# Kernel tuning notes

Hardware: AMD Instinct MI355X
Metric: run time of the kernel (lower is better)

Reference implementation:

```python
import jax, jax.numpy as jnp
import numpy as np

D = 1024
H = 16
HD = D // H
FF = 4 * D
EPS = 1e-5


def setup_inputs() -> dict:
    key = jax.random.key(0)
    ks = jax.random.split(key, 16)
    s = lambda k, shape, scale: jax.random.normal(k, shape, dtype=jnp.float32) * scale
    inp = {
        "x": s(ks[0], (8, 1024, D), 1.0),
        "Wq": s(ks[1], (D, D), D ** -0.5), "bq": jnp.zeros((D,), jnp.float32),
        "Wk": s(ks[2], (D, D), D ** -0.5), "bk": jnp.zeros((D,), jnp.float32),
        "Wv": s(ks[3], (D, D), D ** -0.5), "bv": jnp.zeros((D,), jnp.float32),
        "Wo": s(ks[4], (D, D), D ** -0.5), "bo": jnp.zeros((D,), jnp.float32),
        "W1": s(ks[5], (D, FF), D ** -0.5), "b1": jnp.zeros((FF,), jnp.float32),
        "W2": s(ks[6], (FF, D), FF ** -0.5), "b2": jnp.zeros((D,), jnp.float32),
        "g1": jnp.ones((D,), jnp.float32), "be1": jnp.zeros((D,), jnp.float32),
        "g2": jnp.ones((D,), jnp.float32), "be2": jnp.zeros((D,), jnp.float32),
    }
    return inp


def _layernorm(x, g, b):
    mu = jnp.mean(x, axis=-1, keepdims=True)
    var = jnp.var(x, axis=-1, keepdims=True)
    return (x - mu) * jax.lax.rsqrt(var + EPS) * g + b


def reference(x, Wq, bq, Wk, bk, Wv, bv, Wo, bo, W1, b1, W2, b2, g1, be1, g2, be2):
    B, S, _ = x.shape
    # --- pre-norm attention block (dropout = identity in eval) ---
    h = _layernorm(x, g1, be1)
    q = (h @ Wq + bq).reshape(B, S, H, HD)
    k = (h @ Wk + bk).reshape(B, S, H, HD)
    v = (h @ Wv + bv).reshape(B, S, H, HD)
    scores = jnp.einsum('bqhd,bkhd->bhqk', q, k) / jnp.sqrt(jnp.float32(HD))
    attn = jax.nn.softmax(scores, axis=-1)
    ctx = jnp.einsum('bhqk,bkhd->bqhd', attn, v).reshape(B, S, D)
    x = x + (ctx @ Wo + bo)
    # --- pre-norm FFN block ---
    h = _layernorm(x, g2, be2)
    h = jax.nn.gelu(h @ W1 + b1, approximate=False)
    x = x + (h @ W2 + b2)
    return x
```

## Files before the change

kernel.cpp:

```cpp
#include <hip/hip_runtime.h>
#include <hip/hip_bf16.h>
#include <math.h>
#include <stdint.h>

typedef unsigned short u16;
typedef unsigned int u32;
typedef __attribute__((ext_vector_type(8))) short short8;
typedef __attribute__((ext_vector_type(4))) float f32x4;

__device__ __forceinline__ float b2f(u16 u) {
  union { u32 i; float f; } v; v.i = ((u32)u) << 16; return v.f;
}
__device__ __forceinline__ u16 f2b(float f) {
  union { float f; u32 i; } v; v.f = f;
  return (u16)((v.i + 0x7FFFu + ((v.i >> 16) & 1u)) >> 16);
}

__device__ __forceinline__ void gload_lds16(const u16* g, u16* l) {
  __builtin_amdgcn_global_load_lds((const __attribute__((address_space(1))) void*)g,
                                   (__attribute__((address_space(3))) void*)l, 16, 0, 0);
}

__global__ __launch_bounds__(256) void transpose_k(const float* __restrict__ in,
                                                   u16* __restrict__ out, int K, int N) {
  __shared__ u16 tile[32][33];
  int n0 = blockIdx.x * 32, k0 = blockIdx.y * 32;
  int tx = threadIdx.x & 31, ty = threadIdx.x >> 5;
  #pragma unroll
  for (int i = ty; i < 32; i += 8)
    tile[i][tx] = f2b(in[(size_t)(k0 + i) * N + n0 + tx]);
  __syncthreads();
  #pragma unroll
  for (int i = ty; i < 32; i += 8)
    out[(size_t)(n0 + i) * K + k0 + tx] = tile[tx][i];
}

__global__ __launch_bounds__(256) void vtrans_k(const u16* __restrict__ v, u16* __restrict__ vt) {
  __shared__ u16 tile[32][33];
  int bh = blockIdx.y, b = bh >> 4, h = bh & 15;
  int s0 = (blockIdx.x & 31) * 32, d0 = (blockIdx.x >> 5) * 32;
  int tx = threadIdx.x & 31, ty = threadIdx.x >> 5;
  #pragma unroll
  for (int i = ty; i < 32; i += 8)
    tile[i][tx] = v[(size_t)(b * 1024 + s0 + i) * 1024 + h * 64 + d0 + tx];
  __syncthreads();
  #pragma unroll
  for (int i = ty; i < 32; i += 8)
    vt[(size_t)(bh * 64 + d0 + i) * 1024 + s0 + tx] = tile[tx][i];
}

template<int FP32IN>
__global__ __launch_bounds__(256) void ln_k(const void* __restrict__ xv, const float* __restrict__ g,
                                            const float* __restrict__ be, u16* __restrict__ out) {
  int row = blockIdx.x, t = threadIdx.x;
  float f0, f1, f2, f3;
  if (FP32IN) {
    const float* xr = (const float*)xv + (size_t)row * 1024;
    float4 x4 = *(const float4*)(xr + t * 4);
    f0 = x4.x; f1 = x4.y; f2 = x4.z; f3 = x4.w;
  } else {
    const u16* xr = (const u16*)xv + (size_t)row * 1024;
    ushort4 x4 = *(const ushort4*)(xr + t * 4);
    f0 = b2f(x4.x); f1 = b2f(x4.y); f2 = b2f(x4.z); f3 = b2f(x4.w);
  }
  float s = f0 + f1 + f2 + f3;
  float ss = f0 * f0 + f1 * f1 + f2 * f2 + f3 * f3;
  #pragma unroll
  for (int off = 32; off > 0; off >>= 1) { s += __shfl_down(s, off); ss += __shfl_down(ss, off); }
  __shared__ float sb[4], ssb[4];
  if ((t & 63) == 0) { sb[t >> 6] = s; ssb[t >> 6] = ss; }
  __syncthreads();
  s = sb[0] + sb[1] + sb[2] + sb[3];
  ss = ssb[0] + ssb[1] + ssb[2] + ssb[3];
  float mu = s * (1.0f / 1024.0f);
  float var = ss * (1.0f / 1024.0f) - mu * mu;
  float rstd = rsqrtf(var + 1e-5f);
  float4 gv = *(const float4*)(g + t * 4);
  float4 bv = *(const float4*)(be + t * 4);
  ushort4 o;
  o.x = f2b((f0 - mu) * rstd * gv.x + bv.x);
  o.y = f2b((f1 - mu) * rstd * gv.y + bv.y);
  o.z = f2b((f2 - mu) * rstd * gv.z + bv.z);
  o.w = f2b((f3 - mu) * rstd * gv.w + bv.w);
  *(ushort4*)(out + (size_t)row * 1024 + t * 4) = o;
}

template<int ACT, int RESID, int OUTF32>
__global__ __launch_bounds__(256) void gemm_k(const u16* __restrict__ A, const u16* __restrict__ Bt,
                                              const float* __restrict__ bias, const void* __restrict__ resid,
                                              void* __restrict__ Cv, int M, int N, int K) {
  __shared__ u16 As[2][128 * 32];
  __shared__ u16 Bs[2][128 * 32];
  int n0 = blockIdx.x * 128, m0 = blockIdx.y * 128;
  int t = threadIdx.x;
  int wave = t >> 6, lane = t & 63, quad = lane >> 4, l16 = lane & 15;
  int wm = (wave >> 1) * 64, wn = (wave & 1) * 64;
  f32x4 acc[4][4] = {};
  int lr = lane >> 2;
  int lc = (lane & 3) ^ (lr & 3);
  const u16* Ab = A + (size_t)(m0 + wave * 16 + lr) * K + lc * 8;
  const u16* Bb = Bt + (size_t)(n0 + wave * 16 + lr) * K + lc * 8;
  const int lb = wave * 16 * 32;
  const int rdoff = (quad ^ (l16 & 3)) * 8;
  #pragma unroll
  for (int i = 0; i < 2; i++) {
    gload_lds16(Ab + (size_t)i * 64 * K, &As[0][lb + i * 64 * 32]);
    gload_lds16(Bb + (size_t)i * 64 * K, &Bs[0][lb + i * 64 * 32]);
  }
  const int niter = K >> 5;
  for (int c = 0; c < niter; c++) {
    int buf = c & 1;
    __syncthreads();
    if (c + 1 < niter) {
      int k1 = (c + 1) << 5;
      #pragma unroll
      for (int i = 0; i < 2; i++) {
        gload_lds16(Ab + k1 + (size_t)i * 64 * K, &As[buf ^ 1][lb + i * 64 * 32]);
        gload_lds16(Bb + k1 + (size_t)i * 64 * K, &Bs[buf ^ 1][lb + i * 64 * 32]);
      }
    }
    short8 a[4], b[4];
    #pragma unroll
    for (int i = 0; i < 4; i++)
      a[i] = *(const short8*)(&As[buf][(wm + i * 16 + l16) * 32 + rdoff]);
    #pragma unroll
    for (int j = 0; j < 4; j++)
      b[j] = *(const short8*)(&Bs[buf][(wn + j * 16 + l16) * 32 + rdoff]);
    #pragma unroll
    for (int i = 0; i < 4; i++)
      #pragma unroll
      for (int j = 0; j < 4; j++)
        acc[i][j] = __builtin_amdgcn_mfma_f32_16x16x32_bf16(a[i], b[j], acc[i][j], 0, 0, 0);
  }
  float bcol[4];
  #pragma unroll
  for (int j = 0; j < 4; j++) bcol[j] = bias[n0 + wn + j * 16 + l16];
  #pragma unroll
  for (int i = 0; i < 4; i++) {
    #pragma unroll
    for (int r = 0; r < 4; r++) {
      int row = m0 + wm + i * 16 + quad * 4 + r;
      #pragma unroll
      for (int j = 0; j < 4; j++) {
        int col = n0 + wn + j * 16 + l16;
        float v = acc[i][j][r] + bcol[j];
        if (ACT == 1) {
          float e = v * (2.3022082f + 0.1029431f * v * v);
          float tt = exp2f(fminf(e, 80.0f));
          v = v * tt / (tt + 1.0f);
        }
        if (RESID == 1) v += b2f(((const u16*)resid)[(size_t)row * N + col]);
        if (RESID == 2) v += ((const float*)resid)[(size_t)row * N + col];
        if (OUTF32) ((float*)Cv)[(size_t)row * N + col] = v;
        else        ((u16*)Cv)[(size_t)row * N + col] = f2b(v);
      }
    }
  }
}

__global__ __launch_bounds__(256) void attn_k(const u16* __restrict__ Q, const u16* __restrict__ Kb,
                                              const u16* __restrict__ VT, u16* __restrict__ ctx) {
  int bh = blockIdx.x;
  int b = bh >> 4;
  int q0 = blockIdx.y * 64;
  int t = threadIdx.x, wave = t >> 6, lane = t & 63, quad = lane >> 4, l16 = lane & 15;
  __shared__ u16 Ks[2][64 * 64];
  __shared__ u16 Vs[2][64 * 64];
  __shared__ u16 Plds[4][16][72];
  const size_t base = ((size_t)b * 1024) * 1024 + (size_t)(bh & 15) * 64;
  const u16* Kbase = Kb + base;
  const u16* vtb = VT + (size_t)bh * 64 * 1024;
  int lrow = lane >> 3;
  int lchunk = (lane & 7) ^ (lrow & 7);
  int srow = wave * 16;
  short8 qa[2];
  #pragma unroll
  for (int kh = 0; kh < 2; kh++)
    qa[kh] = *(const short8*)(Q + base + (size_t)(q0 + wave * 16 + l16) * 1024 + kh * 32 + quad * 8);
  #pragma unroll
  for (int half = 0; half < 2; half++) {
    int r8 = srow + half * 8;
    gload_lds16(Kbase + (size_t)(r8 + lrow) * 1024 + lchunk * 8, &Ks[0][r8 * 64]);
    gload_lds16(vtb + (size_t)(r8 + lrow) * 1024 + lchunk * 8, &Vs[0][r8 * 64]);
  }
  f32x4 o[4] = {};
  float l_acc[4] = {0.f, 0.f, 0.f, 0.f};
  for (int c = 0; c < 16; c++) {
    int buf = c & 1;
    __syncthreads();
    if (c < 15) {
      #pragma unroll
      for (int half = 0; half < 2; half++) {
        int r8 = srow + half * 8;
        gload_lds16(Kbase + (size_t)((c + 1) * 64 + r8 + lrow) * 1024 + lchunk * 8, &Ks[buf ^ 1][r8 * 64]);
        gload_lds16(vtb + (size_t)(r8 + lrow) * 1024 + (c + 1) * 64 + lchunk * 8, &Vs[buf ^ 1][r8 * 64]);
      }
    }
    f32x4 s[4] = {};
    #pragma unroll
    for (int kh = 0; kh < 2; kh++)
      #pragma unroll
      for (int j = 0; j < 4; j++) {
        int row = j * 16 + l16;
        int pc = (kh * 4 + quad) ^ (row & 7);
        short8 kb = *(const short8*)(&Ks[buf][row * 64 + pc * 8]);
        s[j] = __builtin_amdgcn_mfma_f32_16x16x32_bf16(qa[kh], kb, s[j], 0, 0, 0);
      }
    #pragma unroll
    for (int j = 0; j < 4; j++)
      #pragma unroll
      for (int r = 0; r < 4; r++) {
        float p = exp2f(s[j][r] * 0.18033688011112042f);
        l_acc[r] += p;
        Plds[wave][quad * 4 + r][j * 16 + l16] = f2b(p);
      }
    #pragma unroll
    for (int kh = 0; kh < 2; kh++) {
      short8 pa = *(const short8*)(&Plds[wave][l16][kh * 32 + quad * 8]);
      #pragma unroll
      for (int d4 = 0; d4 < 4; d4++) {
        int row = d4 * 16 + l16;
        int pc = (kh * 4 + quad) ^ (row & 7);
        short8 vb = *(const short8*)(&Vs[buf][row * 64 + pc * 8]);
        o[d4] = __builtin_amdgcn_mfma_f32_16x16x32_bf16(pa, vb, o[d4], 0, 0, 0);
      }
    }
  }
  #pragma unroll
  for (int off = 1; off < 16; off <<= 1)
    #pragma unroll
    for (int r = 0; r < 4; r++) l_acc[r] += __shfl_xor(l_acc[r], off);
  #pragma unroll
  for (int r = 0; r < 4; r++) {
    float inv = 1.0f / l_acc[r];
    size_t row = (size_t)b * 1024 + q0 + wave * 16 + quad * 4 + r;
    #pragma unroll
    for (int d4 = 0; d4 < 4; d4++) {
      int col = (bh & 15) * 64 + d4 * 16 + l16;
      ctx[row * 1024 + col] = f2b(o[d4][r] * inv);
    }
  }
}

extern "C" void kernel_launch(void* const* d_in, const int* in_sizes, int n_in,
                              void* d_out, int out_size, void* d_ws, size_t ws_size,
                              hipStream_t stream) {
  const float* x   = (const float*)d_in[0];
  const float* Wq  = (const float*)d_in[1];  const float* bq  = (const float*)d_in[2];
  const float* Wk  = (const float*)d_in[3];  const float* bk  = (const float*)d_in[4];
  const float* Wv  = (const float*)d_in[5];  const float* bv  = (const float*)d_in[6];
  const float* Wo  = (const float*)d_in[7];  const float* bo  = (const float*)d_in[8];
  const float* W1  = (const float*)d_in[9];  const float* b1  = (const float*)d_in[10];
  const float* W2  = (const float*)d_in[11]; const float* b2  = (const float*)d_in[12];
  const float* g1  = (const float*)d_in[13]; const float* be1 = (const float*)d_in[14];
  const float* g2  = (const float*)d_in[15]; const float* be2 = (const float*)d_in[16];

  char* ws = (char*)d_ws;
  const size_t MB = 1024 * 1024;
  const bool full = ws_size >= 144 * MB;
  u16* R0  = (u16*)(ws + 0 * MB);
  u16* R1  = (u16*)(ws + 16 * MB);
  u16* R2  = (u16*)(ws + 32 * MB);
  u16* WqT = (u16*)(ws + 48 * MB);
  u16* WkT = (u16*)(ws + 50 * MB);
  u16* WvT = (u16*)(ws + 52 * MB);
  u16* WoT = (u16*)(ws + 54 * MB);
  u16* W1T = full ? (u16*)(ws + 64 * MB) : (u16*)(ws + 56 * MB);
  u16* W2T = full ? (u16*)(ws + 72 * MB) : R2;
  u16* h3f = (u16*)(ws + 80 * MB);
  float* out = (float*)d_out;
  u16* vb  = (u16*)d_out;
  u16* ctx = (u16*)d_out;
  u16* h2  = full ? R2 : (u16*)d_out + (size_t)8192 * 1024;
  u16* vt  = R0;

  transpose_k<<<dim3(32, 32), 256, 0, stream>>>(Wq, WqT, 1024, 1024);
  transpose_k<<<dim3(32, 32), 256, 0, stream>>>(Wk, WkT, 1024, 1024);
  transpose_k<<<dim3(32, 32), 256, 0, stream>>>(Wv, WvT, 1024, 1024);
  transpose_k<<<dim3(32, 32), 256, 0, stream>>>(Wo, WoT, 1024, 1024);
  transpose_k<<<dim3(128, 32), 256, 0, stream>>>(W1, W1T, 1024, 4096);
  if (full) transpose_k<<<dim3(32, 128), 256, 0, stream>>>(W2, W2T, 4096, 1024);

  ln_k<1><<<8192, 256, 0, stream>>>(x, g1, be1, R0);

  gemm_k<0, 0, 0><<<dim3(8, 64), 256, 0, stream>>>(R0, WqT, bq, nullptr, R1, 8192, 1024, 1024);
  gemm_k<0, 0, 0><<<dim3(8, 64), 256, 0, stream>>>(R0, WkT, bk, nullptr, R2, 8192, 1024, 1024);
  gemm_k<0, 0, 0><<<dim3(8, 64), 256, 0, stream>>>(R0, WvT, bv, nullptr, vb, 8192, 1024, 1024);

  vtrans_k<<<dim3(64, 128), 256, 0, stream>>>(vb, vt);

  attn_k<<<dim3(128, 16), 256, 0, stream>>>(R1, R2, vt, ctx);

  gemm_k<0, 2, 0><<<dim3(8, 64), 256, 0, stream>>>(ctx, WoT, bo, x, R1, 8192, 1024, 1024);

  if (!full) transpose_k<<<dim3(32, 128), 256, 0, stream>>>(W2, W2T, 4096, 1024);

  ln_k<0><<<8192, 256, 0, stream>>>(R1, g2, be2, h2);

  if (full) {
    gemm_k<1, 0, 0><<<dim3(32, 64), 256, 0, stream>>>(h2, W1T, b1, nullptr, h3f, 8192, 4096, 1024);
    gemm_k<0, 1, 1><<<dim3(8, 64), 256, 0, stream>>>(h3f, W2T, b2, R1, out, 8192, 1024, 4096);
  } else {
    for (int m = 0; m < 4; m++) {
      const u16* h2c = h2 + (size_t)m * 2048 * 1024;
      const u16* x1c = R1 + (size_t)m * 2048 * 1024;
      float* outc = out + (size_t)m * 2048 * 1024;
      gemm_k<1, 0, 0><<<dim3(32, 16), 256, 0, stream>>>(h2c, W1T, b1, nullptr, R0, 2048, 4096, 1024);
      gemm_k<0, 1, 1><<<dim3(8, 16), 256, 0, stream>>>(R0, W2T, b2, x1c, outc, 2048, 1024, 4096);
    }
  }

  (void)in_sizes; (void)n_in; (void)out_size; (void)ws_size;
}
```

Baseline: 576.3 us.

## Fuse QKV projections into one GEMM and add XCD-aware block remapping

Concatenates Wq/Wk/Wv into a single transposed weight and the three biases into one vector, so the QKV projection becomes one 8192x3072 GEMM writing an interleaved buffer that attention and the V-transpose read with stride 3072. The GEMM now remaps its linear block index so that groups of 8 consecutive blocks land on different M tiles, which is meant to improve L2 locality across the XCDs. The workspace-size fallback path is dropped and the full-size FFN GEMMs always run, which assumes the workspace is large enough. This removes two GEMM launches and extra reads of the LN output, but the strided Q/K loads in attention may be less cache-friendly.

```diff
diff --git a/kernel.cpp b/kernel.cpp
--- a/kernel.cpp
+++ b/kernel.cpp
@@ -35,14 +35,20 @@
     out[(size_t)(n0 + i) * K + k0 + tx] = tile[tx][i];
 }
 
-__global__ __launch_bounds__(256) void vtrans_k(const u16* __restrict__ v, u16* __restrict__ vt) {
+__global__ __launch_bounds__(256) void cat3_k(const float* __restrict__ a, const float* __restrict__ b,
+                                              const float* __restrict__ c, float* __restrict__ o) {
+  int i = blockIdx.x * 256 + threadIdx.x;
+  o[i] = i < 1024 ? a[i] : (i < 2048 ? b[i - 1024] : c[i - 2048]);
+}
+
+__global__ __launch_bounds__(256) void vtrans_k(const u16* __restrict__ qkv, u16* __restrict__ vt) {
   __shared__ u16 tile[32][33];
   int bh = blockIdx.y, b = bh >> 4, h = bh & 15;
   int s0 = (blockIdx.x & 31) * 32, d0 = (blockIdx.x >> 5) * 32;
   int tx = threadIdx.x & 31, ty = threadIdx.x >> 5;
   #pragma unroll
   for (int i = ty; i < 32; i += 8)
-    tile[i][tx] = v[(size_t)(b * 1024 + s0 + i) * 1024 + h * 64 + d0 + tx];
+    tile[i][tx] = qkv[(size_t)(b * 1024 + s0 + i) * 3072 + 2048 + h * 64 + d0 + tx];
   __syncthreads();
   #pragma unroll
   for (int i = ty; i < 32; i += 8)
@@ -88,10 +94,15 @@
 template<int ACT, int RESID, int OUTF32>
 __global__ __launch_bounds__(256) void gemm_k(const u16* __restrict__ A, const u16* __restrict__ Bt,
                                               const float* __restrict__ bias, const void* __restrict__ resid,
-                                              void* __restrict__ Cv, int M, int N, int K) {
+                                              void* __restrict__ Cv, int M, int N, int K, int ldc) {
   __shared__ u16 As[2][128 * 32];
   __shared__ u16 Bs[2][128 * 32];
-  int n0 = blockIdx.x * 128, m0 = blockIdx.y * 128;
+  int Ny = N >> 7;
+  int lin = blockIdx.y * 64 + blockIdx.x;
+  int c8 = lin & 7, sblk = lin >> 3;
+  int mq = sblk / Ny;
+  int m0 = ((mq << 3) | c8) << 7;
+  int n0 = (sblk - mq * Ny) << 7;
   int t = threadIdx.x;
   int wave = t >> 6, lane = t & 63, quad = lane >> 4, l16 = lane & 15;
   int wm = (wave >> 1) * 64, wn = (wave & 1) * 64;
@@ -151,15 +162,15 @@
         }
         if (RESID == 1) v += b2f(((const u16*)resid)[(size_t)row * N + col]);
         if (RESID == 2) v += ((const float*)resid)[(size_t)row * N + col];
-        if (OUTF32) ((float*)Cv)[(size_t)row * N + col] = v;
-        else        ((u16*)Cv)[(size_t)row * N + col] = f2b(v);
-      }
-    }
-  }
-}
-
-__global__ __launch_bounds__(256) void attn_k(const u16* __restrict__ Q, const u16* __restrict__ Kb,
-                                              const u16* __restrict__ VT, u16* __restrict__ ctx) {
+        if (OUTF32) ((float*)Cv)[(size_t)row * ldc + col] = v;
+        else        ((u16*)Cv)[(size_t)row * ldc + col] = f2b(v);
+      }
+    }
+  }
+}
+
+__global__ __launch_bounds__(256) void attn_k(const u16* __restrict__ QKV, const u16* __restrict__ VT,
+                                              u16* __restrict__ ctx) {
   int bh = blockIdx.x;
   int b = bh >> 4;
   int q0 = blockIdx.y * 64;
@@ -167,8 +178,8 @@
   __shared__ u16 Ks[2][64 * 64];
   __shared__ u16 Vs[2][64 * 64];
   __shared__ u16 Plds[4][16][72];
-  const size_t base = ((size_t)b * 1024) * 1024 + (size_t)(bh & 15) * 64;
-  const u16* Kbase = Kb + base;
+  const size_t base = ((size_t)b * 1024) * 3072 + (size_t)(bh & 15) * 64;
+  const u16* Kbase = QKV + base + 1024;
   const u16* vtb = VT + (size_t)bh * 64 * 1024;
   int lrow = lane >> 3;
   int lchunk = (lane & 7) ^ (lrow & 7);
@@ -176,11 +187,11 @@
   short8 qa[2];
   #pragma unroll
   for (int kh = 0; kh < 2; kh++)
-    qa[kh] = *(const short8*)(Q + base + (size_t)(q0 + wave * 16 + l16) * 1024 + kh * 32 + quad * 8);
+    qa[kh] = *(const short8*)(QKV + base + (size_t)(q0 + wave * 16 + l16) * 3072 + kh * 32 + quad * 8);
   #pragma unroll
   for (int half = 0; half < 2; half++) {
     int r8 = srow + half * 8;
-    gload_lds16(Kbase + (size_t)(r8 + lrow) * 1024 + lchunk * 8, &Ks[0][r8 * 64]);
+    gload_lds16(Kbase + (size_t)(r8 + lrow) * 3072 + lchunk * 8, &Ks[0][r8 * 64]);
     gload_lds16(vtb + (size_t)(r8 + lrow) * 1024 + lchunk * 8, &Vs[0][r8 * 64]);
   }
   f32x4 o[4] = {};
@@ -192,7 +203,7 @@
       #pragma unroll
       for (int half = 0; half < 2; half++) {
         int r8 = srow + half * 8;
-        gload_lds16(Kbase + (size_t)((c + 1) * 64 + r8 + lrow) * 1024 + lchunk * 8, &Ks[buf ^ 1][r8 * 64]);
+        gload_lds16(Kbase + (size_t)((c + 1) * 64 + r8 + lrow) * 3072 + lchunk * 8, &Ks[buf ^ 1][r8 * 64]);
         gload_lds16(vtb + (size_t)(r8 + lrow) * 1024 + (c + 1) * 64 + lchunk * 8, &Vs[buf ^ 1][r8 * 64]);
       }
     }
@@ -257,58 +268,47 @@
 
   char* ws = (char*)d_ws;
   const size_t MB = 1024 * 1024;
-  const bool full = ws_size >= 144 * MB;
-  u16* R0  = (u16*)(ws + 0 * MB);
-  u16* R1  = (u16*)(ws + 16 * MB);
-  u16* R2  = (u16*)(ws + 32 * MB);
-  u16* WqT = (u16*)(ws + 48 * MB);
-  u16* WkT = (u16*)(ws + 50 * MB);
-  u16* WvT = (u16*)(ws + 52 * MB);
-  u16* WoT = (u16*)(ws + 54 * MB);
-  u16* W1T = full ? (u16*)(ws + 64 * MB) : (u16*)(ws + 56 * MB);
-  u16* W2T = full ? (u16*)(ws + 72 * MB) : R2;
-  u16* h3f = (u16*)(ws + 80 * MB);
+  u16* h1    = (u16*)(ws + 0 * MB);
+  u16* qkv   = (u16*)(ws + 16 * MB);
+  u16* x1    = (u16*)(ws + 16 * MB);
+  u16* h2    = (u16*)(ws + 32 * MB);
+  u16* W2T   = (u16*)(ws + 48 * MB);
+  u16* WqkvT = (u16*)(ws + 64 * MB);
+  u16* WoT   = (u16*)(ws + 70 * MB);
+  u16* W1T   = (u16*)(ws + 72 * MB);
+  float* bqkv = (float*)(ws + 80 * MB);
+  u16* h3f   = (u16*)(ws + 80 * MB);
+  u16* vt    = h1;
+  u16* ctx   = (u16*)d_out;
   float* out = (float*)d_out;
-  u16* vb  = (u16*)d_out;
-  u16* ctx = (u16*)d_out;
-  u16* h2  = full ? R2 : (u16*)d_out + (size_t)8192 * 1024;
-  u16* vt  = R0;
-
-  transpose_k<<<dim3(32, 32), 256, 0, stream>>>(Wq, WqT, 1024, 1024);
-  transpose_k<<<dim3(32, 32), 256, 0, stream>>>(Wk, WkT, 1024, 1024);
-  transpose_k<<<dim3(32, 32), 256, 0, stream>>>(Wv, WvT, 1024, 1024);
+
+  transpose_k<<<dim3(32, 32), 256, 0, stream>>>(Wq, WqkvT, 1024, 1024);
+  transpose_k<<<dim3(32, 32), 256, 0, stream>>>(Wk, WqkvT + (size_t)1024 * 1024, 1024, 1024);
+  transpose_k<<<dim3(32, 32), 256, 0, stream>>>(Wv, WqkvT + (size_t)2048 * 1024, 1024, 1024);
   transpose_k<<<dim3(32, 32), 256, 0, stream>>>(Wo, WoT, 1024, 1024);
   transpose_k<<<dim3(128, 32), 256, 0, stream>>>(W1, W1T, 1024, 4096);
-  if (full) transpose_k<<<dim3(32, 128), 256, 0, stream>>>(W2, W2T, 4096, 1024);
-
-  ln_k<1><<<8192, 256, 0, stream>>>(x, g1, be1, R0);
-
-  gemm_k<0, 0, 0><<<dim3(8, 64), 256, 0, stream>>>(R0, WqT, bq, nullptr, R1, 8192, 1024, 1024);
-  gemm_k<0, 0, 0><<<dim3(8, 64), 256, 0, stream>>>(R0, WkT, bk, nullptr, R2, 8192, 1024, 1024);
-  gemm_k<0, 0, 0><<<dim3(8, 64), 256, 0, stream>>>(R0, WvT, bv, nullptr, vb, 8192, 1024, 1024);
-
-  vtrans_k<<<dim3(64, 128), 256, 0, stream>>>(vb, vt);
-
-  attn_k<<<dim3(128, 16), 256, 0, stream>>>(R1, R2, vt, ctx);
-
-  gemm_k<0, 2, 0><<<dim3(8, 64), 256, 0, stream>>>(ctx, WoT, bo, x, R1, 8192, 1024, 1024);
-
-  if (!full) transpose_k<<<dim3(32, 128), 256, 0, stream>>>(W2, W2T, 4096, 1024);
-
-  ln_k<0><<<8192, 256, 0, stream>>>(R1, g2, be2, h2);
-
-  if (full) {
-    gemm_k<1, 0, 0><<<dim3(32, 64), 256, 0, stream>>>(h2, W1T, b1, nullptr, h3f, 8192, 4096, 1024);
-    gemm_k<0, 1, 1><<<dim3(8, 64), 256, 0, stream>>>(h3f, W2T, b2, R1, out, 8192, 1024, 4096);
-  } else {
-    for (int m = 0; m < 4; m++) {
-      const u16* h2c = h2 + (size_t)m * 2048 * 1024;
-      const u16* x1c = R1 + (size_t)m * 2048 * 1024;
-      float* outc = out + (size_t)m * 2048 * 1024;
-      gemm_k<1, 0, 0><<<dim3(32, 16), 256, 0, stream>>>(h2c, W1T, b1, nullptr, R0, 2048, 4096, 1024);
-      gemm_k<0, 1, 1><<<dim3(8, 16), 256, 0, stream>>>(R0, W2T, b2, x1c, outc, 2048, 1024, 4096);
-    }
-  }
+  cat3_k<<<12, 256, 0, stream>>>(bq, bk, bv, bqkv);
+
+  ln_k<1><<<8192, 256, 0, stream>>>(x, g1, be1, h1);
+
+  gemm_k<0, 0, 0><<<dim3(64, 24), 256, 0, stream>>>(h1, WqkvT, bqkv, nullptr, qkv,
+                                                    8192, 3072, 1024, 3072);
+
+  vtrans_k<<<dim3(64, 128), 256, 0, stream>>>(qkv, vt);
+
+  attn_k<<<dim3(128, 16), 256, 0, stream>>>(qkv, vt, ctx);
+
+  gemm_k<0, 2, 0><<<dim3(64, 8), 256, 0, stream>>>(ctx, WoT, bo, x, x1,
+                                                   8192, 1024, 1024, 1024);
+
+  transpose_k<<<dim3(32, 128), 256, 0, stream>>>(W2, W2T, 4096, 1024);
+
+  ln_k<0><<<8192, 256, 0, stream>>>(x1, g2, be2, h2);
+
+  gemm_k<1, 0, 0><<<dim3(64, 32), 256, 0, stream>>>(h2, W1T, b1, nullptr, h3f,
+                                                    8192, 4096, 1024, 4096);
+  gemm_k<0, 1, 1><<<dim3(64, 8), 256, 0, stream>>>(h3f, W2T, b2, x1, out,
+                                                   8192, 1024, 4096, 1024);
 
   (void)in_sizes; (void)n_in; (void)out_size; (void)ws_size;
 }
```

Measured after the change: 542.0 us. -6.0%, faster.
